# Optimization experiments

Hardware: AMD Instinct MI355X
Metric: run time of the kernel (lower is better)

Reference implementation:

```python
import jax, jax.numpy as jnp
import numpy as np

N_BITS = 8
N_LEVELS = 2 ** N_BITS  # 256
MAX_ITERS = 10
BIG = 3.0e38  # stand-in for +inf that stays finite in fp32


def _init_scales(x):
    """Replicates init_quantization_scale: iteratively peel off 3-sigma outliers.
    Returns per-iteration (thresholds, deltas, zero_points, valid) arrays of
    length MAX_ITERS; `valid[i]` marks iterations that actually recorded a group
    (torch's `break` on empty non-zero set)."""
    xf = x.reshape(-1)

    def step(carry, _):
        xc, done = carry
        absx = jnp.abs(xc)
        nz = xc != 0.0
        n = jnp.sum(nz)
        active = jnp.logical_and(jnp.logical_not(done), n > 0)
        nf = jnp.maximum(n, 1).astype(xc.dtype)
        # mean / unbiased variance of |non-zero elements| (torch .mean()/.var())
        mean = jnp.sum(jnp.where(nz, absx, 0.0)) / nf
        var = jnp.sum(jnp.where(nz, (absx - mean) ** 2, 0.0)) / jnp.maximum(nf - 1.0, 1.0)
        thr = mean + 3.0 * jnp.sqrt(var)
        max_abs = jnp.max(absx)
        # if thr > max: inliers = non-zero elements; else inliers = ~outliers (zeros included)
        inlier = jnp.where(thr > max_abs, nz, absx <= thr)
        x_min = jnp.min(jnp.where(inlier, xc, jnp.asarray(BIG, xc.dtype)))
        x_max = jnp.max(jnp.where(inlier, xc, jnp.asarray(-BIG, xc.dtype)))
        delta = (x_max - x_min) / (N_LEVELS - 1)
        zp = jnp.round(-x_min / delta)
        # keep only outliers for the next iteration
        xc_next = jnp.where(active, jnp.where(absx > thr, xc, 0.0), xc)
        done_next = jnp.logical_or(done, n == 0)
        return (xc_next, done_next), (thr, delta, zp, active)

    (_, _), (thrs, deltas, zps, valids) = jax.lax.scan(
        step, (xf, jnp.asarray(False)), None, length=MAX_ITERS)
    return thrs, deltas, zps, valids


def _dequant(x, thrs, deltas, zps, valids):
    absx = jnp.abs(x)
    # group index: band i is (thr[i-1], thr[i]]; band 0 contributes 0 as in torch
    gi = jnp.zeros(x.shape, dtype=jnp.int32)
    for i in range(1, MAX_ITERS):  # static, small loop over groups
        band = (absx > thrs[i - 1]) & (absx <= thrs[i]) & valids[i]
        gi = gi + band.astype(jnp.int32) * i
    n_groups = jnp.sum(valids.astype(jnp.int32))
    gi = jnp.clip(gi, 0, jnp.maximum(n_groups - 1, 0))
    d = deltas[gi]   # per-element scale
    z = zps[gi]      # per-element zero point
    x_q = jnp.clip(jnp.round(x / d) + z, 0.0, float(N_LEVELS - 1))
    return (x_q - z) * d


def setup_inputs() -> dict:
    key = jax.random.key(0)
    x = jax.random.normal(key, (4, 4096, 4096), dtype=jnp.float32)
    return {"x": x}


def reference(x):
    thrs, deltas, zps, valids = _init_scales(x)
    return _dequant(x, thrs, deltas, zps, valids)
```

## Files before the change

kernel.cpp:

```cpp
#include <hip/hip_runtime.h>

#define BIGF 3.402823466e38f
#define LCAP 2048u
#define NB   2048
#define NT   256

typedef float f32x4 __attribute__((ext_vector_type(4)));

struct State {
  double sum0, sumsq0;
  double sum1, sumsq1;
  double sum2, sumsq2;
  unsigned n0, n1, n2;
  float maxabs0, minnz0, maxnz0;
  float maxabs1, minnz1, maxnz1;
  float maxabs2, minnz2, maxnz2;
  float bmin0, bmax0;
  float bmin1, bmax1;
  unsigned count1, count2;
  float thr0f, thr1f;
  int special0;
  float thr[10], delta[10], zp[10];
  int valid[10];
};

__device__ inline void atomicMinF(float* addr, float v) {
  unsigned* ua = (unsigned*)addr;
  unsigned cur = *ua;
  while (v < __uint_as_float(cur)) {
    unsigned prev = atomicCAS(ua, cur, __float_as_uint(v));
    if (prev == cur) break;
    cur = prev;
  }
}
__device__ inline void atomicMaxF(float* addr, float v) {
  unsigned* ua = (unsigned*)addr;
  unsigned cur = *ua;
  while (v > __uint_as_float(cur)) {
    unsigned prev = atomicCAS(ua, cur, __float_as_uint(v));
    if (prev == cur) break;
    cur = prev;
  }
}

struct Acc8 {
  double sum, sumsq;
  unsigned cnt;
  float maxabs, minnz, maxnz, bmin, bmax;
};
__device__ inline void acc_init(Acc8& a) {
  a.sum = 0.0; a.sumsq = 0.0; a.cnt = 0u;
  a.maxabs = 0.0f;
  a.minnz = BIGF; a.maxnz = -BIGF;
  a.bmin = BIGF; a.bmax = -BIGF;
}
__device__ inline void acc_merge(Acc8& a, const Acc8& b) {
  a.sum += b.sum; a.sumsq += b.sumsq; a.cnt += b.cnt;
  a.maxabs = fmaxf(a.maxabs, b.maxabs);
  a.minnz = fminf(a.minnz, b.minnz); a.maxnz = fmaxf(a.maxnz, b.maxnz);
  a.bmin = fminf(a.bmin, b.bmin);   a.bmax = fmaxf(a.bmax, b.bmax);
}
__device__ inline void acc_wave_reduce(Acc8& a) {
  #pragma unroll
  for (int off = 32; off > 0; off >>= 1) {
    a.sum    += __shfl_down(a.sum, off);
    a.sumsq  += __shfl_down(a.sumsq, off);
    a.cnt    += __shfl_down(a.cnt, off);
    a.maxabs = fmaxf(a.maxabs, __shfl_down(a.maxabs, off));
    a.minnz  = fminf(a.minnz,  __shfl_down(a.minnz, off));
    a.maxnz  = fmaxf(a.maxnz,  __shfl_down(a.maxnz, off));
    a.bmin   = fminf(a.bmin,   __shfl_down(a.bmin, off));
    a.bmax   = fmaxf(a.bmax,   __shfl_down(a.bmax, off));
  }
}
template <int NWAVES>
__device__ inline bool acc_block_reduce(Acc8& a, Acc8* s_part) {
  __syncthreads();
  acc_wave_reduce(a);
  int tid = threadIdx.x;
  if ((tid & 63) == 0) s_part[tid >> 6] = a;
  __syncthreads();
  if (tid == 0) {
    #pragma unroll
    for (int w = 1; w < NWAVES; ++w) acc_merge(a, s_part[w]);
    return true;
  }
  return false;
}

__device__ inline float compute_thr(double sum, double sumsq, unsigned n) {
  double nf = (double)(n > 0u ? n : 1u);
  double mean = sum / nf;
  double nm1 = nf - 1.0; if (nm1 < 1.0) nm1 = 1.0;
  double var = (sumsq - sum * sum / nf) / nm1;
  if (var < 0.0) var = 0.0;
  return (float)(mean + 3.0 * sqrt(var));
}

__device__ inline void finalize_group(float thr, float maxabs, unsigned n,
                                      float minnz, float maxnz, float bmin, float bmax,
                                      bool clampZero, float* dOut, float* zOut, int* vOut) {
  float xmin, xmax;
  if (thr > maxabs) { xmin = minnz; xmax = maxnz; }
  else {
    xmin = bmin; xmax = bmax;
    if (clampZero) { xmin = fminf(xmin, 0.0f); xmax = fmaxf(xmax, 0.0f); }
  }
  float d = (xmax - xmin) / 255.0f;
  int v = (n > 0u) ? 1 : 0;
  float z;
  if (v && d > 0.0f && d < BIGF) { z = rintf((-xmin) / d); }
  else { d = 1.0f; z = 0.0f; }
  *dOut = d; *zOut = z; *vOut = v;
}

__device__ inline void stat1(float f, Acc8& a) {
  float ab = fabsf(f);
  bool nz = (f != 0.0f);
  a.cnt += nz ? 1u : 0u;
  double dab = (double)ab;
  a.sum += dab; a.sumsq += dab * dab;
  a.maxabs = fmaxf(a.maxabs, ab);
  a.minnz = fminf(a.minnz, nz ? f : BIGF);
  a.maxnz = fmaxf(a.maxnz, nz ? f : -BIGF);
}

__global__ void __launch_bounds__(256) k1_stats(const float* __restrict__ x, long long n,
                                                Acc8* __restrict__ part) {
  __shared__ Acc8 s_part[4];
  Acc8 a[4];
  #pragma unroll
  for (int u = 0; u < 4; ++u) acc_init(a[u]);
  const f32x4* x4 = (const f32x4*)x;
  long long n4 = n >> 2;
  long long tid = (long long)blockIdx.x * NT + threadIdx.x;
  long long nthreads = (long long)gridDim.x * NT;
  long long step = nthreads * 8;
  long long nfull = (n4 / step) * step;
  for (long long i = (long long)blockIdx.x * (NT * 8) + threadIdx.x; i < nfull; i += step) {
    f32x4 v[8];
    #pragma unroll
    for (int u = 0; u < 8; ++u) v[u] = x4[i + u * NT];
    #pragma unroll
    for (int u = 0; u < 8; ++u) {
      stat1(v[u].x, a[u & 3]); stat1(v[u].y, a[u & 3]);
      stat1(v[u].z, a[u & 3]); stat1(v[u].w, a[u & 3]);
    }
  }
  for (long long i = nfull + tid; i < n4; i += nthreads) {
    f32x4 v = x4[i];
    stat1(v.x, a[0]); stat1(v.y, a[0]); stat1(v.z, a[0]); stat1(v.w, a[0]);
  }
  for (long long i = (n4 << 2) + tid; i < n; i += nthreads) stat1(x[i], a[0]);

  acc_merge(a[0], a[1]); acc_merge(a[2], a[3]); acc_merge(a[0], a[2]);
  if (acc_block_reduce<4>(a[0], s_part)) part[blockIdx.x] = a[0];
}

__global__ void __launch_bounds__(1024) k1r_reduce(State* st, const Acc8* __restrict__ part, int np) {
  __shared__ Acc8 s_part[16];
  Acc8 a; acc_init(a);
  for (int j = threadIdx.x; j < np; j += 1024) acc_merge(a, part[j]);
  if (acc_block_reduce<16>(a, s_part)) {
    st->sum0 = a.sum; st->sumsq0 = a.sumsq; st->n0 = a.cnt;
    st->maxabs0 = a.maxabs; st->minnz0 = a.minnz; st->maxnz0 = a.maxnz;
    float t = compute_thr(a.sum, a.sumsq, a.cnt);
    st->thr0f = t;
    st->special0 = (t > a.maxabs) ? 1 : 0;
    st->count1 = 0u; st->count2 = 0u;
    st->bmin1 = BIGF; st->bmax1 = -BIGF;
    st->sum2 = 0.0; st->sumsq2 = 0.0; st->n2 = 0u;
    st->maxabs2 = a.maxabs; st->minnz2 = BIGF; st->maxnz2 = -BIGF;
  }
}

__device__ inline void proc2(float f, unsigned idx, float thr0, bool special, Acc8& a,
                             unsigned* l_cnt, float2* l_buf,
                             State* st, float2* __restrict__ buf1, unsigned cap1) {
  float ab = fabsf(f);
  bool out = ab > thr0;
  bool inl = special ? (f != 0.0f) : (!out);
  a.bmin = fminf(a.bmin, inl ? f : BIGF);
  a.bmax = fmaxf(a.bmax, inl ? f : -BIGF);
  a.cnt += out ? 1u : 0u;
  double dab = out ? (double)ab : 0.0;
  a.sum += dab; a.sumsq += dab * dab;
  a.minnz = fminf(a.minnz, out ? f : BIGF);
  a.maxnz = fmaxf(a.maxnz, out ? f : -BIGF);
  unsigned long long m = __ballot(out);
  if (m) {
    unsigned lo = (unsigned)m, hi = (unsigned)(m >> 32);
    int pw = (int)__builtin_amdgcn_mbcnt_hi(hi, __builtin_amdgcn_mbcnt_lo(lo, 0u));
    int nout = __builtin_popcountll(m);
    int leader = __builtin_ctzll(m);
    unsigned bbase = 0u;
    if ((int)(threadIdx.x & 63) == leader) bbase = atomicAdd(l_cnt, (unsigned)nout);
    bbase = (unsigned)__shfl((int)bbase, leader);
    if (out) {
      unsigned p = bbase + (unsigned)pw;
      float2 rec = make_float2(f, __uint_as_float(idx));
      if (p < LCAP) l_buf[p] = rec;
      else { unsigned g = atomicAdd(&st->count1, 1u); if (g < cap1) buf1[g] = rec; }
    }
  }
}

__global__ void __launch_bounds__(256) k2_pass(const float* __restrict__ x, long long n, State* st,
                                               float2* __restrict__ buf1, unsigned cap1,
                                               Acc8* __restrict__ part) {
  __shared__ Acc8 s_part[4];
  __shared__ float2 l_buf[LCAP];
  __shared__ unsigned l_cnt, l_base, l_m;
  if (threadIdx.x == 0) l_cnt = 0u;
  __syncthreads();

  float thr0 = st->thr0f;
  bool special = st->special0 != 0;

  Acc8 a0, a1; acc_init(a0); acc_init(a1);
  const f32x4* x4 = (const f32x4*)x;
  long long n4 = n >> 2;
  long long tid = (long long)blockIdx.x * NT + threadIdx.x;
  long long nthreads = (long long)gridDim.x * NT;
  long long step = nthreads * 4;
  long long nfull = (n4 / step) * step;
  for (long long i = (long long)blockIdx.x * (NT * 4) + threadIdx.x; i < nfull; i += step) {
    f32x4 v0 = x4[i];
    f32x4 v1 = x4[i + NT];
    f32x4 v2 = x4[i + 2 * NT];
    f32x4 v3 = x4[i + 3 * NT];
    unsigned b0 = (unsigned)(i) << 2, b1 = (unsigned)(i + NT) << 2,
             b2 = (unsigned)(i + 2 * NT) << 2, b3 = (unsigned)(i + 3 * NT) << 2;
    proc2(v0.x, b0 + 0u, thr0, special, a0, &l_cnt, l_buf, st, buf1, cap1);
    proc2(v0.y, b0 + 1u, thr0, special, a0, &l_cnt, l_buf, st, buf1, cap1);
    proc2(v0.z, b0 + 2u, thr0, special, a0, &l_cnt, l_buf, st, buf1, cap1);
    proc2(v0.w, b0 + 3u, thr0, special, a0, &l_cnt, l_buf, st, buf1, cap1);
    proc2(v1.x, b1 + 0u, thr0, special, a0, &l_cnt, l_buf, st, buf1, cap1);
    proc2(v1.y, b1 + 1u, thr0, special, a0, &l_cnt, l_buf, st, buf1, cap1);
    proc2(v1.z, b1 + 2u, thr0, special, a0, &l_cnt, l_buf, st, buf1, cap1);
    proc2(v1.w, b1 + 3u, thr0, special, a0, &l_cnt, l_buf, st, buf1, cap1);
    proc2(v2.x, b2 + 0u, thr0, special, a1, &l_cnt, l_buf, st, buf1, cap1);
    proc2(v2.y, b2 + 1u, thr0, special, a1, &l_cnt, l_buf, st, buf1, cap1);
    proc2(v2.z, b2 + 2u, thr0, special, a1, &l_cnt, l_buf, st, buf1, cap1);
    proc2(v2.w, b2 + 3u, thr0, special, a1, &l_cnt, l_buf, st, buf1, cap1);
    proc2(v3.x, b3 + 0u, thr0, special, a1, &l_cnt, l_buf, st, buf1, cap1);
    proc2(v3.y, b3 + 1u, thr0, special, a1, &l_cnt, l_buf, st, buf1, cap1);
    proc2(v3.z, b3 + 2u, thr0, special, a1, &l_cnt, l_buf, st, buf1, cap1);
    proc2(v3.w, b3 + 3u, thr0, special, a1, &l_cnt, l_buf, st, buf1, cap1);
  }
  for (long long i = nfull + tid; i < n4; i += nthreads) {
    f32x4 v = x4[i];
    unsigned b = (unsigned)(i) << 2;
    proc2(v.x, b + 0u, thr0, special, a0, &l_cnt, l_buf, st, buf1, cap1);
    proc2(v.y, b + 1u, thr0, special, a0, &l_cnt, l_buf, st, buf1, cap1);
    proc2(v.z, b + 2u, thr0, special, a0, &l_cnt, l_buf, st, buf1, cap1);
    proc2(v.w, b + 3u, thr0, special, a0, &l_cnt, l_buf, st, buf1, cap1);
  }
  for (long long i = (n4 << 2) + tid; i < n; i += nthreads) {
    proc2(x[i], (unsigned)i, thr0, special, a0, &l_cnt, l_buf, st, buf1, cap1);
  }

  __syncthreads();
  if (threadIdx.x == 0) {
    l_m = l_cnt < LCAP ? l_cnt : LCAP;
    l_base = atomicAdd(&st->count1, l_m);
  }
  __syncthreads();
  for (unsigned i = threadIdx.x; i < l_m; i += NT) {
    unsigned g = l_base + i;
    if (g < cap1) buf1[g] = l_buf[i];
  }
  acc_merge(a0, a1);
  if (acc_block_reduce<4>(a0, s_part)) part[blockIdx.x] = a0;
}

__global__ void __launch_bounds__(1024) k2r_reduce(State* st, const Acc8* __restrict__ part, int np) {
  __shared__ Acc8 s_part[16];
  Acc8 a; acc_init(a);
  for (int j = threadIdx.x; j < np; j += 1024) acc_merge(a, part[j]);
  if (acc_block_reduce<16>(a, s_part)) {
    st->bmin0 = a.bmin; st->bmax0 = a.bmax;
    st->sum1 = a.sum; st->sumsq1 = a.sumsq; st->n1 = a.cnt;
    st->maxabs1 = st->maxabs0;
    st->minnz1 = a.minnz; st->maxnz1 = a.maxnz;
    st->thr1f = compute_thr(a.sum, a.sumsq, a.cnt);
  }
}

__global__ void __launch_bounds__(256) k3_pass(State* st, const float2* __restrict__ buf1, unsigned cap1,
                                               float* __restrict__ buf2, unsigned cap2) {
  __shared__ Acc8 s_part[4];
  __shared__ float l_buf[LCAP];
  __shared__ unsigned l_cnt, l_base, l_m;
  if (threadIdx.x == 0) l_cnt = 0u;
  __syncthreads();

  unsigned c1 = st->count1; if (c1 > cap1) c1 = cap1;
  float thr1 = st->thr1f;

  Acc8 a; acc_init(a);
  unsigned stride = gridDim.x * blockDim.x;
  for (unsigned j = blockIdx.x * blockDim.x + threadIdx.x; j < c1; j += stride) {
    float f = buf1[j].x;
    float ab = fabsf(f);
    if (ab <= thr1) { a.bmin = fminf(a.bmin, f); a.bmax = fmaxf(a.bmax, f); }
    else {
      a.cnt++; a.sum += (double)ab; a.sumsq += (double)ab * (double)ab;
      a.minnz = fminf(a.minnz, f); a.maxnz = fmaxf(a.maxnz, f);
      unsigned p = atomicAdd(&l_cnt, 1u);
      if (p < LCAP) l_buf[p] = f;
      else { unsigned g = atomicAdd(&st->count2, 1u); if (g < cap2) buf2[g] = f; }
    }
  }
  __syncthreads();
  if (threadIdx.x == 0) {
    l_m = l_cnt < LCAP ? l_cnt : LCAP;
    l_base = atomicAdd(&st->count2, l_m);
  }
  __syncthreads();
  for (unsigned i = threadIdx.x; i < l_m; i += blockDim.x) {
    unsigned g = l_base + i;
    if (g < cap2) buf2[g] = l_buf[i];
  }
  if (acc_block_reduce<4>(a, s_part)) {
    atomicMinF(&st->bmin1, a.bmin); atomicMaxF(&st->bmax1, a.bmax);
    atomicAdd(&st->sum2, a.sum); atomicAdd(&st->sumsq2, a.sumsq); atomicAdd(&st->n2, a.cnt);
    atomicMinF(&st->minnz2, a.minnz); atomicMaxF(&st->maxnz2, a.maxnz);
  }
}

__global__ void __launch_bounds__(1024) k4_finalize(State* st, const float* __restrict__ buf2, unsigned cap2) {
  __shared__ Acc8 s_part[16];
  __shared__ float sh_thr[10], sh_delta[10], sh_zp[10];
  __shared__ int sh_valid[10];
  __shared__ double sh_sum, sh_sumsq;
  __shared__ unsigned sh_n;
  __shared__ float sh_maxabs, sh_minnz, sh_maxnz;
  int tid = threadIdx.x;

  if (tid == 0) {
    float thr0 = compute_thr(st->sum0, st->sumsq0, st->n0);
    sh_thr[0] = thr0;
    finalize_group(thr0, st->maxabs0, st->n0, st->minnz0, st->maxnz0,
                   st->bmin0, st->bmax0, false,
                   &sh_delta[0], &sh_zp[0], &sh_valid[0]);
    float thr1 = compute_thr(st->sum1, st->sumsq1, st->n1);
    sh_thr[1] = thr1;
    finalize_group(thr1, st->maxabs1, st->n1, st->minnz1, st->maxnz1,
                   st->bmin1, st->bmax1, true,
                   &sh_delta[1], &sh_zp[1], &sh_valid[1]);
    sh_sum = st->sum2; sh_sumsq = st->sumsq2; sh_n = st->n2;
    sh_maxabs = st->maxabs2; sh_minnz = st->minnz2; sh_maxnz = st->maxnz2;
  }
  __syncthreads();
  unsigned c2 = st->count2; if (c2 > cap2) c2 = cap2;

  for (int i = 2; i < 10; ++i) {
    if (tid == 0) sh_thr[i] = compute_thr(sh_sum, sh_sumsq, sh_n);
    __syncthreads();
    float tp = sh_thr[i - 1], tc = sh_thr[i];
    Acc8 a; acc_init(a);
    for (unsigned j = tid; j < c2; j += 1024u) {
      float f = buf2[j];
      float ab = fabsf(f);
      if (ab > tp && ab <= tc) { a.bmin = fminf(a.bmin, f); a.bmax = fmaxf(a.bmax, f); }
      if (ab > tc) {
        a.cnt++; a.sum += (double)ab; a.sumsq += (double)ab * (double)ab;
        a.maxabs = fmaxf(a.maxabs, ab);
        a.minnz = fminf(a.minnz, f); a.maxnz = fmaxf(a.maxnz, f);
      }
    }
    if (acc_block_reduce<16>(a, s_part)) {
      finalize_group(tc, sh_maxabs, sh_n, sh_minnz, sh_maxnz, a.bmin, a.bmax,
                     true, &sh_delta[i], &sh_zp[i], &sh_valid[i]);
      if (sh_n > 0u) {
        sh_sum = a.sum; sh_sumsq = a.sumsq; sh_n = a.cnt;
        sh_maxabs = a.maxabs; sh_minnz = a.minnz; sh_maxnz = a.maxnz;
      }
    }
    __syncthreads();
  }
  if (tid < 10) {
    st->thr[tid] = sh_thr[tid]; st->delta[tid] = sh_delta[tid];
    st->zp[tid] = sh_zp[tid];   st->valid[tid] = sh_valid[tid];
  }
}

__device__ inline float dq0(float v, float d0, float z0) {
  float q = rintf(v / d0) + z0;
  q = fminf(fmaxf(q, 0.0f), 255.0f);
  return (q - z0) * d0;
}

__global__ void __launch_bounds__(256) k5_dequant(const float* __restrict__ x, float* __restrict__ out,
                                                  long long n, const State* __restrict__ st) {
  float d0 = st->delta[0], z0 = st->zp[0];
  const f32x4* x4 = (const f32x4*)x;
  f32x4* o4 = (f32x4*)out;
  long long n4 = n >> 2;
  long long tid = (long long)blockIdx.x * NT + threadIdx.x;
  long long nthreads = (long long)gridDim.x * NT;
  long long step = nthreads * 8;
  long long nfull = (n4 / step) * step;
  for (long long i = (long long)blockIdx.x * (NT * 8) + threadIdx.x; i < nfull; i += step) {
    f32x4 v[8];
    #pragma unroll
    for (int u = 0; u < 8; ++u) v[u] = x4[i + u * NT];
    #pragma unroll
    for (int u = 0; u < 8; ++u) {
      f32x4 o;
      o.x = dq0(v[u].x, d0, z0);
      o.y = dq0(v[u].y, d0, z0);
      o.z = dq0(v[u].z, d0, z0);
      o.w = dq0(v[u].w, d0, z0);
      __builtin_nontemporal_store(o, &o4[i + u * NT]);
    }
  }
  for (long long i = nfull + tid; i < n4; i += nthreads) {
    f32x4 v = x4[i];
    f32x4 o;
    o.x = dq0(v.x, d0, z0); o.y = dq0(v.y, d0, z0);
    o.z = dq0(v.z, d0, z0); o.w = dq0(v.w, d0, z0);
    o4[i] = o;
  }
  for (long long i = (n4 << 2) + tid; i < n; i += nthreads) {
    out[i] = dq0(x[i], d0, z0);
  }
}

__device__ inline float dq1(float v, const float* thr, const float* dl, const float* zp, const int* vld) {
  float ab = fabsf(v);
  float d = dl[0], z = zp[0];
  #pragma unroll
  for (int i = 1; i < 10; ++i) {
    bool band = (vld[i] != 0) && (ab > thr[i - 1]) && (ab <= thr[i]);
    d = band ? dl[i] : d;
    z = band ? zp[i] : z;
  }
  float q = rintf(v / d) + z;
  q = fminf(fmaxf(q, 0.0f), 255.0f);
  return (q - z) * d;
}

__global__ void __launch_bounds__(256) k6_outliers(const float2* __restrict__ buf1, unsigned cap1,
                                                   float* __restrict__ out, const State* __restrict__ st) {
  unsigned c1 = st->count1; if (c1 > cap1) c1 = cap1;
  float thr[10], dl[10], zp[10]; int vld[10];
  #pragma unroll
  for (int i = 0; i < 10; ++i) {
    thr[i] = st->thr[i]; dl[i] = st->delta[i]; zp[i] = st->zp[i]; vld[i] = st->valid[i];
  }
  unsigned stride = gridDim.x * blockDim.x;
  for (unsigned j = blockIdx.x * blockDim.x + threadIdx.x; j < c1; j += stride) {
    float2 rec = buf1[j];
    out[__float_as_uint(rec.y)] = dq1(rec.x, thr, dl, zp, vld);
  }
}

extern "C" void kernel_launch(void* const* d_in, const int* in_sizes, int n_in,
                              void* d_out, int out_size, void* d_ws, size_t ws_size,
                              hipStream_t stream) {
  const float* x = (const float*)d_in[0];
  float* out = (float*)d_out;
  long long n = (long long)in_sizes[0];

  char* p = (char*)d_ws;
  State* st = (State*)p;            p += 4096;
  Acc8* part1 = (Acc8*)p;           p += (size_t)NB * sizeof(Acc8);
  Acc8* part2 = (Acc8*)p;           p += (size_t)NB * sizeof(Acc8);
  size_t used = (size_t)(p - (char*)d_ws);
  used = (used + 255) & ~(size_t)255;
  size_t avail = ws_size > used ? ws_size - used : 0;
  size_t cap2_sz = avail / 8;
  if (cap2_sz > (size_t)(1u << 20) * 4) cap2_sz = (size_t)(1u << 20) * 4;
  unsigned cap2 = (unsigned)(cap2_sz / 4);
  float* buf2 = (float*)((char*)d_ws + used);
  float2* buf1 = (float2*)(buf2 + cap2);
  unsigned cap1 = (unsigned)((avail - (size_t)cap2 * 4) / 8);

  hipLaunchKernelGGL(k1_stats,    dim3(NB),  dim3(NT),   0, stream, x, n, part1);
  hipLaunchKernelGGL(k1r_reduce,  dim3(1),   dim3(1024), 0, stream, st, (const Acc8*)part1, NB);
  hipLaunchKernelGGL(k2_pass,     dim3(NB),  dim3(NT),   0, stream, x, n, st, buf1, cap1, part2);
  hipLaunchKernelGGL(k2r_reduce,  dim3(1),   dim3(1024), 0, stream, st, (const Acc8*)part2, NB);
  hipLaunchKernelGGL(k3_pass,     dim3(256), dim3(NT),   0, stream, st, (const float2*)buf1, cap1, buf2, cap2);
  hipLaunchKernelGGL(k4_finalize, dim3(1),   dim3(1024), 0, stream, st, (const float*)buf2, cap2);
  hipLaunchKernelGGL(k5_dequant,  dim3(NB),  dim3(NT),   0, stream, x, out, n, st);
  hipLaunchKernelGGL(k6_outliers, dim3(512), dim3(NT),   0, stream, (const float2*)buf1, cap1, out, st);
}
```

Baseline: 676.6 us.

## Fuse first two passes via sampled speculative threshold with fallback pass

The first stats pass now estimates a conservative threshold from a local sample in each block. It captures every element above that estimate into a compact buffer while also collecting inlier min/max, which removes the second full read of the input. If the true threshold falls below any block's estimate, or the buffer overflows, a fallback kernel redoes the full pass. The outlier scatter kernel is folded into the dequant kernel through a wave-uniform fast/slow path. Index-carrying records shrink to plain floats. The cost is extra ballot/LDS work in the first pass and a correctness dependence on the speculative threshold check.

```diff
diff --git a/kernel.cpp b/kernel.cpp
--- a/kernel.cpp
+++ b/kernel.cpp
@@ -17,9 +17,12 @@
   float maxabs2, minnz2, maxnz2;
   float bmin0, bmax0;
   float bmin1, bmax1;
-  unsigned count1, count2;
-  float thr0f, thr1f;
+  unsigned countA;
+  unsigned count1;
+  unsigned count2;
+  float thr0f;
   int special0;
+  int fallback;
   float thr[10], delta[10], zp[10];
   int valid[10];
 };
@@ -48,6 +51,8 @@
   unsigned cnt;
   float maxabs, minnz, maxnz, bmin, bmax;
 };
+struct AccP { Acc8 a; float tspec; };
+
 __device__ inline void acc_init(Acc8& a) {
   a.sum = 0.0; a.sumsq = 0.0; a.cnt = 0u;
   a.maxabs = 0.0f;
@@ -114,7 +119,13 @@
   *dOut = d; *zOut = z; *vOut = v;
 }
 
-__device__ inline void stat1(float f, Acc8& a) {
+__global__ void k0_init(State* st) {
+  if (threadIdx.x == 0 && blockIdx.x == 0) st->countA = 0u;
+}
+
+__device__ inline void proc1(float f, float tspec, Acc8& a,
+                             unsigned* l_cnt, float* l_buf,
+                             State* st, float* __restrict__ bufA, unsigned capA) {
   float ab = fabsf(f);
   bool nz = (f != 0.0f);
   a.cnt += nz ? 1u : 0u;
@@ -123,70 +134,9 @@
   a.maxabs = fmaxf(a.maxabs, ab);
   a.minnz = fminf(a.minnz, nz ? f : BIGF);
   a.maxnz = fmaxf(a.maxnz, nz ? f : -BIGF);
-}
-
-__global__ void __launch_bounds__(256) k1_stats(const float* __restrict__ x, long long n,
-                                                Acc8* __restrict__ part) {
-  __shared__ Acc8 s_part[4];
-  Acc8 a[4];
-  #pragma unroll
-  for (int u = 0; u < 4; ++u) acc_init(a[u]);
-  const f32x4* x4 = (const f32x4*)x;
-  long long n4 = n >> 2;
-  long long tid = (long long)blockIdx.x * NT + threadIdx.x;
-  long long nthreads = (long long)gridDim.x * NT;
-  long long step = nthreads * 8;
-  long long nfull = (n4 / step) * step;
-  for (long long i = (long long)blockIdx.x * (NT * 8) + threadIdx.x; i < nfull; i += step) {
-    f32x4 v[8];
-    #pragma unroll
-    for (int u = 0; u < 8; ++u) v[u] = x4[i + u * NT];
-    #pragma unroll
-    for (int u = 0; u < 8; ++u) {
-      stat1(v[u].x, a[u & 3]); stat1(v[u].y, a[u & 3]);
-      stat1(v[u].z, a[u & 3]); stat1(v[u].w, a[u & 3]);
-    }
-  }
-  for (long long i = nfull + tid; i < n4; i += nthreads) {
-    f32x4 v = x4[i];
-    stat1(v.x, a[0]); stat1(v.y, a[0]); stat1(v.z, a[0]); stat1(v.w, a[0]);
-  }
-  for (long long i = (n4 << 2) + tid; i < n; i += nthreads) stat1(x[i], a[0]);
-
-  acc_merge(a[0], a[1]); acc_merge(a[2], a[3]); acc_merge(a[0], a[2]);
-  if (acc_block_reduce<4>(a[0], s_part)) part[blockIdx.x] = a[0];
-}
-
-__global__ void __launch_bounds__(1024) k1r_reduce(State* st, const Acc8* __restrict__ part, int np) {
-  __shared__ Acc8 s_part[16];
-  Acc8 a; acc_init(a);
-  for (int j = threadIdx.x; j < np; j += 1024) acc_merge(a, part[j]);
-  if (acc_block_reduce<16>(a, s_part)) {
-    st->sum0 = a.sum; st->sumsq0 = a.sumsq; st->n0 = a.cnt;
-    st->maxabs0 = a.maxabs; st->minnz0 = a.minnz; st->maxnz0 = a.maxnz;
-    float t = compute_thr(a.sum, a.sumsq, a.cnt);
-    st->thr0f = t;
-    st->special0 = (t > a.maxabs) ? 1 : 0;
-    st->count1 = 0u; st->count2 = 0u;
-    st->bmin1 = BIGF; st->bmax1 = -BIGF;
-    st->sum2 = 0.0; st->sumsq2 = 0.0; st->n2 = 0u;
-    st->maxabs2 = a.maxabs; st->minnz2 = BIGF; st->maxnz2 = -BIGF;
-  }
-}
-
-__device__ inline void proc2(float f, unsigned idx, float thr0, bool special, Acc8& a,
-                             unsigned* l_cnt, float2* l_buf,
-                             State* st, float2* __restrict__ buf1, unsigned cap1) {
-  float ab = fabsf(f);
-  bool out = ab > thr0;
-  bool inl = special ? (f != 0.0f) : (!out);
-  a.bmin = fminf(a.bmin, inl ? f : BIGF);
-  a.bmax = fmaxf(a.bmax, inl ? f : -BIGF);
-  a.cnt += out ? 1u : 0u;
-  double dab = out ? (double)ab : 0.0;
-  a.sum += dab; a.sumsq += dab * dab;
-  a.minnz = fminf(a.minnz, out ? f : BIGF);
-  a.maxnz = fmaxf(a.maxnz, out ? f : -BIGF);
+  bool out = ab > tspec;
+  a.bmin = fminf(a.bmin, out ? BIGF : f);
+  a.bmax = fmaxf(a.bmax, out ? -BIGF : f);
   unsigned long long m = __ballot(out);
   if (m) {
     unsigned lo = (unsigned)m, hi = (unsigned)(m >> 32);
@@ -198,68 +148,194 @@
     bbase = (unsigned)__shfl((int)bbase, leader);
     if (out) {
       unsigned p = bbase + (unsigned)pw;
-      float2 rec = make_float2(f, __uint_as_float(idx));
-      if (p < LCAP) l_buf[p] = rec;
-      else { unsigned g = atomicAdd(&st->count1, 1u); if (g < cap1) buf1[g] = rec; }
-    }
-  }
-}
-
-__global__ void __launch_bounds__(256) k2_pass(const float* __restrict__ x, long long n, State* st,
-                                               float2* __restrict__ buf1, unsigned cap1,
-                                               Acc8* __restrict__ part) {
+      if (p < LCAP) l_buf[p] = f;
+      else { unsigned g = atomicAdd(&st->countA, 1u); if (g < capA) bufA[g] = f; }
+    }
+  }
+}
+
+__global__ void __launch_bounds__(256) k1_stats(const float* __restrict__ x, long long n,
+                                                AccP* __restrict__ part,
+                                                float* __restrict__ bufA, unsigned capA,
+                                                State* st) {
   __shared__ Acc8 s_part[4];
-  __shared__ float2 l_buf[LCAP];
+  __shared__ float l_buf[LCAP];
+  __shared__ unsigned l_cnt, l_base, l_m;
+  __shared__ float s_s[4], s_ss[4], s_c[4], s_tspec;
+  int tid = threadIdx.x;
+  if (tid == 0) l_cnt = 0u;
+
+  const f32x4* x4 = (const f32x4*)x;
+  long long n4 = n >> 2;
+  long long gtid = (long long)blockIdx.x * NT + tid;
+  long long nthreads = (long long)gridDim.x * NT;
+  long long step = nthreads * 8;
+  long long nfull = (n4 / step) * step;
+  long long i0 = (long long)blockIdx.x * (NT * 8) + tid;
+
+  {
+    float s = 0.0f, ss = 0.0f; unsigned c = 0u;
+    #pragma unroll
+    for (int u = 0; u < 2; ++u) {
+      long long i = i0 + u * NT;
+      if (i < n4) {
+        f32x4 v = x4[i];
+        float e[4] = {v.x, v.y, v.z, v.w};
+        #pragma unroll
+        for (int k = 0; k < 4; ++k) {
+          float ab = fabsf(e[k]);
+          c += (ab != 0.0f) ? 1u : 0u;
+          s += ab; ss += ab * ab;
+        }
+      }
+    }
+    #pragma unroll
+    for (int off = 32; off > 0; off >>= 1) {
+      s  += __shfl_down(s, off);
+      ss += __shfl_down(ss, off);
+      c  += __shfl_down(c, off);
+    }
+    if ((tid & 63) == 0) { s_s[tid >> 6] = s; s_ss[tid >> 6] = ss; s_c[tid >> 6] = (float)c; }
+    __syncthreads();
+    if (tid == 0) {
+      float S = s_s[0] + s_s[1] + s_s[2] + s_s[3];
+      float SS = s_ss[0] + s_ss[1] + s_ss[2] + s_ss[3];
+      float C = s_c[0] + s_c[1] + s_c[2] + s_c[3];
+      float nf = C > 1.0f ? C : 1.0f;
+      float m = S / nf;
+      float var = (SS - S * S / nf) / fmaxf(nf - 1.0f, 1.0f);
+      var = fmaxf(var, 0.0f);
+      s_tspec = 0.8f * (m + 3.0f * sqrtf(var));
+    }
+    __syncthreads();
+  }
+  float tspec = s_tspec;
+
+  Acc8 a0, a1; acc_init(a0); acc_init(a1);
+  for (long long i = i0; i < nfull; i += step) {
+    f32x4 v[8];
+    #pragma unroll
+    for (int u = 0; u < 8; ++u) v[u] = x4[i + u * NT];
+    #pragma unroll
+    for (int u = 0; u < 8; ++u) {
+      Acc8& a = (u & 1) ? a1 : a0;
+      proc1(v[u].x, tspec, a, &l_cnt, l_buf, st, bufA, capA);
+      proc1(v[u].y, tspec, a, &l_cnt, l_buf, st, bufA, capA);
+      proc1(v[u].z, tspec, a, &l_cnt, l_buf, st, bufA, capA);
+      proc1(v[u].w, tspec, a, &l_cnt, l_buf, st, bufA, capA);
+    }
+  }
+  for (long long i = nfull + gtid; i < n4; i += nthreads) {
+    f32x4 v = x4[i];
+    proc1(v.x, tspec, a0, &l_cnt, l_buf, st, bufA, capA);
+    proc1(v.y, tspec, a0, &l_cnt, l_buf, st, bufA, capA);
+    proc1(v.z, tspec, a0, &l_cnt, l_buf, st, bufA, capA);
+    proc1(v.w, tspec, a0, &l_cnt, l_buf, st, bufA, capA);
+  }
+  for (long long i = (n4 << 2) + gtid; i < n; i += nthreads) {
+    proc1(x[i], tspec, a0, &l_cnt, l_buf, st, bufA, capA);
+  }
+
+  __syncthreads();
+  if (tid == 0) {
+    l_m = l_cnt < LCAP ? l_cnt : LCAP;
+    l_base = atomicAdd(&st->countA, l_m);
+  }
+  __syncthreads();
+  for (unsigned i = tid; i < l_m; i += NT) {
+    unsigned g = l_base + i;
+    if (g < capA) bufA[g] = l_buf[i];
+  }
+  acc_merge(a0, a1);
+  if (acc_block_reduce<4>(a0, s_part)) { part[blockIdx.x].a = a0; part[blockIdx.x].tspec = tspec; }
+}
+
+__global__ void __launch_bounds__(1024) k1r_reduce(State* st, const AccP* __restrict__ part,
+                                                   int np, unsigned capA) {
+  __shared__ Acc8 s_part[16];
+  __shared__ float s_tm[16];
+  Acc8 a; acc_init(a);
+  float tm = 0.0f;
+  for (int j = threadIdx.x; j < np; j += 1024) {
+    acc_merge(a, part[j].a);
+    tm = fmaxf(tm, part[j].tspec);
+  }
+  #pragma unroll
+  for (int off = 32; off > 0; off >>= 1) tm = fmaxf(tm, __shfl_down(tm, off));
+  if ((threadIdx.x & 63) == 0) s_tm[threadIdx.x >> 6] = tm;
+  if (acc_block_reduce<16>(a, s_part)) {
+    #pragma unroll
+    for (int w = 1; w < 16; ++w) tm = fmaxf(tm, s_tm[w]);
+    st->sum0 = a.sum; st->sumsq0 = a.sumsq; st->n0 = a.cnt;
+    st->maxabs0 = a.maxabs; st->minnz0 = a.minnz; st->maxnz0 = a.maxnz;
+    float t = compute_thr(a.sum, a.sumsq, a.cnt);
+    st->thr0f = t;
+    st->special0 = (t > a.maxabs) ? 1 : 0;
+    unsigned cA = st->countA;
+    bool ok = (tm <= t) && (cA <= capA);
+    st->fallback = ok ? 0 : 1;
+    st->bmin0 = ok ? a.bmin : BIGF;
+    st->bmax0 = ok ? a.bmax : -BIGF;
+    st->count1 = 0u; st->count2 = 0u;
+    st->sum1 = 0.0; st->sumsq1 = 0.0; st->n1 = 0u;
+    st->maxabs1 = a.maxabs;
+    st->minnz1 = BIGF; st->maxnz1 = -BIGF;
+    st->bmin1 = BIGF; st->bmax1 = -BIGF;
+    st->sum2 = 0.0; st->sumsq2 = 0.0; st->n2 = 0u;
+    st->maxabs2 = a.maxabs;
+    st->minnz2 = BIGF; st->maxnz2 = -BIGF;
+  }
+}
+
+__global__ void __launch_bounds__(256) k2_full(const float* __restrict__ x, long long n, State* st,
+                                               float* __restrict__ bufB, unsigned capB) {
+  if (st->fallback == 0) return;
+  __shared__ Acc8 s_part[4];
+  __shared__ float l_buf[LCAP];
   __shared__ unsigned l_cnt, l_base, l_m;
   if (threadIdx.x == 0) l_cnt = 0u;
   __syncthreads();
 
   float thr0 = st->thr0f;
   bool special = st->special0 != 0;
-
-  Acc8 a0, a1; acc_init(a0); acc_init(a1);
+  Acc8 a; acc_init(a);
   const f32x4* x4 = (const f32x4*)x;
   long long n4 = n >> 2;
-  long long tid = (long long)blockIdx.x * NT + threadIdx.x;
+  long long gtid = (long long)blockIdx.x * NT + threadIdx.x;
   long long nthreads = (long long)gridDim.x * NT;
-  long long step = nthreads * 4;
-  long long nfull = (n4 / step) * step;
-  for (long long i = (long long)blockIdx.x * (NT * 4) + threadIdx.x; i < nfull; i += step) {
-    f32x4 v0 = x4[i];
-    f32x4 v1 = x4[i + NT];
-    f32x4 v2 = x4[i + 2 * NT];
-    f32x4 v3 = x4[i + 3 * NT];
-    unsigned b0 = (unsigned)(i) << 2, b1 = (unsigned)(i + NT) << 2,
-             b2 = (unsigned)(i + 2 * NT) << 2, b3 = (unsigned)(i + 3 * NT) << 2;
-    proc2(v0.x, b0 + 0u, thr0, special, a0, &l_cnt, l_buf, st, buf1, cap1);
-    proc2(v0.y, b0 + 1u, thr0, special, a0, &l_cnt, l_buf, st, buf1, cap1);
-    proc2(v0.z, b0 + 2u, thr0, special, a0, &l_cnt, l_buf, st, buf1, cap1);
-    proc2(v0.w, b0 + 3u, thr0, special, a0, &l_cnt, l_buf, st, buf1, cap1);
-    proc2(v1.x, b1 + 0u, thr0, special, a0, &l_cnt, l_buf, st, buf1, cap1);
-    proc2(v1.y, b1 + 1u, thr0, special, a0, &l_cnt, l_buf, st, buf1, cap1);
-    proc2(v1.z, b1 + 2u, thr0, special, a0, &l_cnt, l_buf, st, buf1, cap1);
-    proc2(v1.w, b1 + 3u, thr0, special, a0, &l_cnt, l_buf, st, buf1, cap1);
-    proc2(v2.x, b2 + 0u, thr0, special, a1, &l_cnt, l_buf, st, buf1, cap1);
-    proc2(v2.y, b2 + 1u, thr0, special, a1, &l_cnt, l_buf, st, buf1, cap1);
-    proc2(v2.z, b2 + 2u, thr0, special, a1, &l_cnt, l_buf, st, buf1, cap1);
-    proc2(v2.w, b2 + 3u, thr0, special, a1, &l_cnt, l_buf, st, buf1, cap1);
-    proc2(v3.x, b3 + 0u, thr0, special, a1, &l_cnt, l_buf, st, buf1, cap1);
-    proc2(v3.y, b3 + 1u, thr0, special, a1, &l_cnt, l_buf, st, buf1, cap1);
-    proc2(v3.z, b3 + 2u, thr0, special, a1, &l_cnt, l_buf, st, buf1, cap1);
-    proc2(v3.w, b3 + 3u, thr0, special, a1, &l_cnt, l_buf, st, buf1, cap1);
-  }
-  for (long long i = nfull + tid; i < n4; i += nthreads) {
+  for (long long i = gtid; i < n4; i += nthreads) {
     f32x4 v = x4[i];
-    unsigned b = (unsigned)(i) << 2;
-    proc2(v.x, b + 0u, thr0, special, a0, &l_cnt, l_buf, st, buf1, cap1);
-    proc2(v.y, b + 1u, thr0, special, a0, &l_cnt, l_buf, st, buf1, cap1);
-    proc2(v.z, b + 2u, thr0, special, a0, &l_cnt, l_buf, st, buf1, cap1);
-    proc2(v.w, b + 3u, thr0, special, a0, &l_cnt, l_buf, st, buf1, cap1);
-  }
-  for (long long i = (n4 << 2) + tid; i < n; i += nthreads) {
-    proc2(x[i], (unsigned)i, thr0, special, a0, &l_cnt, l_buf, st, buf1, cap1);
-  }
-
+    float e[4] = {v.x, v.y, v.z, v.w};
+    #pragma unroll
+    for (int k = 0; k < 4; ++k) {
+      float f = e[k];
+      float ab = fabsf(f);
+      bool out = ab > thr0;
+      bool inl = special ? (f != 0.0f) : (!out);
+      if (inl) { a.bmin = fminf(a.bmin, f); a.bmax = fmaxf(a.bmax, f); }
+      if (out) {
+        a.cnt++; a.sum += (double)ab; a.sumsq += (double)ab * (double)ab;
+        a.minnz = fminf(a.minnz, f); a.maxnz = fmaxf(a.maxnz, f);
+        unsigned p = atomicAdd(&l_cnt, 1u);
+        if (p < LCAP) l_buf[p] = f;
+        else { unsigned g = atomicAdd(&st->count1, 1u); if (g < capB) bufB[g] = f; }
+      }
+    }
+  }
+  for (long long i = (n4 << 2) + gtid; i < n; i += nthreads) {
+    float f = x[i];
+    float ab = fabsf(f);
+    bool out = ab > thr0;
+    bool inl = special ? (f != 0.0f) : (!out);
+    if (inl) { a.bmin = fminf(a.bmin, f); a.bmax = fmaxf(a.bmax, f); }
+    if (out) {
+      a.cnt++; a.sum += (double)ab; a.sumsq += (double)ab * (double)ab;
+      a.minnz = fminf(a.minnz, f); a.maxnz = fmaxf(a.maxnz, f);
+      unsigned p = atomicAdd(&l_cnt, 1u);
+      if (p < LCAP) l_buf[p] = f;
+      else { unsigned g = atomicAdd(&st->count1, 1u); if (g < capB) bufB[g] = f; }
+    }
+  }
   __syncthreads();
   if (threadIdx.x == 0) {
     l_m = l_cnt < LCAP ? l_cnt : LCAP;
@@ -268,26 +344,77 @@
   __syncthreads();
   for (unsigned i = threadIdx.x; i < l_m; i += NT) {
     unsigned g = l_base + i;
-    if (g < cap1) buf1[g] = l_buf[i];
-  }
-  acc_merge(a0, a1);
-  if (acc_block_reduce<4>(a0, s_part)) part[blockIdx.x] = a0;
-}
-
-__global__ void __launch_bounds__(1024) k2r_reduce(State* st, const Acc8* __restrict__ part, int np) {
-  __shared__ Acc8 s_part[16];
+    if (g < capB) bufB[g] = l_buf[i];
+  }
+  if (acc_block_reduce<4>(a, s_part)) {
+    atomicMinF(&st->bmin0, a.bmin); atomicMaxF(&st->bmax0, a.bmax);
+    atomicAdd(&st->sum1, a.sum); atomicAdd(&st->sumsq1, a.sumsq); atomicAdd(&st->n1, a.cnt);
+    atomicMinF(&st->minnz1, a.minnz); atomicMaxF(&st->maxnz1, a.maxnz);
+  }
+}
+
+__global__ void __launch_bounds__(256) k2c_pass(State* st, const float* __restrict__ bufA, unsigned capA,
+                                                float* __restrict__ bufB, unsigned capB) {
+  if (st->fallback != 0) return;
+  __shared__ Acc8 s_part[4];
+  __shared__ float l_buf[LCAP];
+  __shared__ unsigned l_cnt, l_base, l_m;
+  if (threadIdx.x == 0) l_cnt = 0u;
+  __syncthreads();
+
+  unsigned cA = st->countA; if (cA > capA) cA = capA;
+  float thr0 = st->thr0f;
   Acc8 a; acc_init(a);
-  for (int j = threadIdx.x; j < np; j += 1024) acc_merge(a, part[j]);
-  if (acc_block_reduce<16>(a, s_part)) {
-    st->bmin0 = a.bmin; st->bmax0 = a.bmax;
-    st->sum1 = a.sum; st->sumsq1 = a.sumsq; st->n1 = a.cnt;
-    st->maxabs1 = st->maxabs0;
-    st->minnz1 = a.minnz; st->maxnz1 = a.maxnz;
-    st->thr1f = compute_thr(a.sum, a.sumsq, a.cnt);
-  }
-}
-
-__global__ void __launch_bounds__(256) k3_pass(State* st, const float2* __restrict__ buf1, unsigned cap1,
+  unsigned stride = gridDim.x * blockDim.x;
+  unsigned cA4 = cA >> 2;
+  const f32x4* bufA4 = (const f32x4*)bufA;
+  for (unsigned j = blockIdx.x * blockDim.x + threadIdx.x; j < cA4; j += stride) {
+    f32x4 v = bufA4[j];
+    float e[4] = {v.x, v.y, v.z, v.w};
+    #pragma unroll
+    for (int k = 0; k < 4; ++k) {
+      float f = e[k];
+      float ab = fabsf(f);
+      if (ab <= thr0) { a.bmin = fminf(a.bmin, f); a.bmax = fmaxf(a.bmax, f); }
+      else {
+        a.cnt++; a.sum += (double)ab; a.sumsq += (double)ab * (double)ab;
+        a.minnz = fminf(a.minnz, f); a.maxnz = fmaxf(a.maxnz, f);
+        unsigned p = atomicAdd(&l_cnt, 1u);
+        if (p < LCAP) l_buf[p] = f;
+        else { unsigned g = atomicAdd(&st->count1, 1u); if (g < capB) bufB[g] = f; }
+      }
+    }
+  }
+  for (unsigned j = (cA4 << 2) + blockIdx.x * blockDim.x + threadIdx.x; j < cA; j += stride) {
+    float f = bufA[j];
+    float ab = fabsf(f);
+    if (ab <= thr0) { a.bmin = fminf(a.bmin, f); a.bmax = fmaxf(a.bmax, f); }
+    else {
+      a.cnt++; a.sum += (double)ab; a.sumsq += (double)ab * (double)ab;
+      a.minnz = fminf(a.minnz, f); a.maxnz = fmaxf(a.maxnz, f);
+      unsigned p = atomicAdd(&l_cnt, 1u);
+      if (p < LCAP) l_buf[p] = f;
+      else { unsigned g = atomicAdd(&st->count1, 1u); if (g < capB) bufB[g] = f; }
+    }
+  }
+  __syncthreads();
+  if (threadIdx.x == 0) {
+    l_m = l_cnt < LCAP ? l_cnt : LCAP;
+    l_base = atomicAdd(&st->count1, l_m);
+  }
+  __syncthreads();
+  for (unsigned i = threadIdx.x; i < l_m; i += NT) {
+    unsigned g = l_base + i;
+    if (g < capB) bufB[g] = l_buf[i];
+  }
+  if (acc_block_reduce<4>(a, s_part)) {
+    atomicMinF(&st->bmin0, a.bmin); atomicMaxF(&st->bmax0, a.bmax);
+    atomicAdd(&st->sum1, a.sum); atomicAdd(&st->sumsq1, a.sumsq); atomicAdd(&st->n1, a.cnt);
+    atomicMinF(&st->minnz1, a.minnz); atomicMaxF(&st->maxnz1, a.maxnz);
+  }
+}
+
+__global__ void __launch_bounds__(256) k3_pass(State* st, const float* __restrict__ bufB, unsigned capB,
                                                float* __restrict__ buf2, unsigned cap2) {
   __shared__ Acc8 s_part[4];
   __shared__ float l_buf[LCAP];
@@ -295,13 +422,13 @@
   if (threadIdx.x == 0) l_cnt = 0u;
   __syncthreads();
 
-  unsigned c1 = st->count1; if (c1 > cap1) c1 = cap1;
-  float thr1 = st->thr1f;
+  unsigned c1 = st->count1; if (c1 > capB) c1 = capB;
+  float thr1 = compute_thr(st->sum1, st->sumsq1, st->n1);
 
   Acc8 a; acc_init(a);
   unsigned stride = gridDim.x * blockDim.x;
   for (unsigned j = blockIdx.x * blockDim.x + threadIdx.x; j < c1; j += stride) {
-    float f = buf1[j].x;
+    float f = bufB[j];
     float ab = fabsf(f);
     if (ab <= thr1) { a.bmin = fminf(a.bmin, f); a.bmax = fmaxf(a.bmax, f); }
     else {
@@ -391,43 +518,6 @@
   q = fminf(fmaxf(q, 0.0f), 255.0f);
   return (q - z0) * d0;
 }
-
-__global__ void __launch_bounds__(256) k5_dequant(const float* __restrict__ x, float* __restrict__ out,
-                                                  long long n, const State* __restrict__ st) {
-  float d0 = st->delta[0], z0 = st->zp[0];
-  const f32x4* x4 = (const f32x4*)x;
-  f32x4* o4 = (f32x4*)out;
-  long long n4 = n >> 2;
-  long long tid = (long long)blockIdx.x * NT + threadIdx.x;
-  long long nthreads = (long long)gridDim.x * NT;
-  long long step = nthreads * 8;
-  long long nfull = (n4 / step) * step;
-  for (long long i = (long long)blockIdx.x * (NT * 8) + threadIdx.x; i < nfull; i += step) {
-    f32x4 v[8];
-    #pragma unroll
-    for (int u = 0; u < 8; ++u) v[u] = x4[i + u * NT];
-    #pragma unroll
-    for (int u = 0; u < 8; ++u) {
-      f32x4 o;
-      o.x = dq0(v[u].x, d0, z0);
-      o.y = dq0(v[u].y, d0, z0);
-      o.z = dq0(v[u].z, d0, z0);
-      o.w = dq0(v[u].w, d0, z0);
-      __builtin_nontemporal_store(o, &o4[i + u * NT]);
-    }
-  }
-  for (long long i = nfull + tid; i < n4; i += nthreads) {
-    f32x4 v = x4[i];
-    f32x4 o;
-    o.x = dq0(v.x, d0, z0); o.y = dq0(v.y, d0, z0);
-    o.z = dq0(v.z, d0, z0); o.w = dq0(v.w, d0, z0);
-    o4[i] = o;
-  }
-  for (long long i = (n4 << 2) + tid; i < n; i += nthreads) {
-    out[i] = dq0(x[i], d0, z0);
-  }
-}
-
 __device__ inline float dq1(float v, const float* thr, const float* dl, const float* zp, const int* vld) {
   float ab = fabsf(v);
   float d = dl[0], z = zp[0];
@@ -441,19 +531,52 @@
   q = fminf(fmaxf(q, 0.0f), 255.0f);
   return (q - z) * d;
 }
-
-__global__ void __launch_bounds__(256) k6_outliers(const float2* __restrict__ buf1, unsigned cap1,
-                                                   float* __restrict__ out, const State* __restrict__ st) {
-  unsigned c1 = st->count1; if (c1 > cap1) c1 = cap1;
+__device__ inline float dq(float v, float t0, float d0, float z0,
+                           const float* thr, const float* dl, const float* zp, const int* vld) {
+  if (__any(fabsf(v) > t0)) return dq1(v, thr, dl, zp, vld);
+  return dq0(v, d0, z0);
+}
+
+__global__ void __launch_bounds__(256) k5_dequant(const float* __restrict__ x, float* __restrict__ out,
+                                                  long long n, const State* __restrict__ st) {
   float thr[10], dl[10], zp[10]; int vld[10];
   #pragma unroll
   for (int i = 0; i < 10; ++i) {
     thr[i] = st->thr[i]; dl[i] = st->delta[i]; zp[i] = st->zp[i]; vld[i] = st->valid[i];
   }
-  unsigned stride = gridDim.x * blockDim.x;
-  for (unsigned j = blockIdx.x * blockDim.x + threadIdx.x; j < c1; j += stride) {
-    float2 rec = buf1[j];
-    out[__float_as_uint(rec.y)] = dq1(rec.x, thr, dl, zp, vld);
+  float d0 = dl[0], z0 = zp[0], t0 = thr[0];
+  const f32x4* x4 = (const f32x4*)x;
+  f32x4* o4 = (f32x4*)out;
+  long long n4 = n >> 2;
+  long long gtid = (long long)blockIdx.x * NT + threadIdx.x;
+  long long nthreads = (long long)gridDim.x * NT;
+  long long step = nthreads * 8;
+  long long nfull = (n4 / step) * step;
+  for (long long i = (long long)blockIdx.x * (NT * 8) + threadIdx.x; i < nfull; i += step) {
+    f32x4 v[8];
+    #pragma unroll
+    for (int u = 0; u < 8; ++u) v[u] = __builtin_nontemporal_load(&x4[i + u * NT]);
+    #pragma unroll
+    for (int u = 0; u < 8; ++u) {
+      f32x4 o;
+      o.x = dq(v[u].x, t0, d0, z0, thr, dl, zp, vld);
+      o.y = dq(v[u].y, t0, d0, z0, thr, dl, zp, vld);
+      o.z = dq(v[u].z, t0, d0, z0, thr, dl, zp, vld);
+      o.w = dq(v[u].w, t0, d0, z0, thr, dl, zp, vld);
+      __builtin_nontemporal_store(o, &o4[i + u * NT]);
+    }
+  }
+  for (long long i = nfull + gtid; i < n4; i += nthreads) {
+    f32x4 v = x4[i];
+    f32x4 o;
+    o.x = dq(v.x, t0, d0, z0, thr, dl, zp, vld);
+    o.y = dq(v.y, t0, d0, z0, thr, dl, zp, vld);
+    o.z = dq(v.z, t0, d0, z0, thr, dl, zp, vld);
+    o.w = dq(v.w, t0, d0, z0, thr, dl, zp, vld);
+    o4[i] = o;
+  }
+  for (long long i = (n4 << 2) + gtid; i < n; i += nthreads) {
+    out[i] = dq(x[i], t0, d0, z0, thr, dl, zp, vld);
   }
 }
 
@@ -466,24 +589,26 @@
 
   char* p = (char*)d_ws;
   State* st = (State*)p;            p += 4096;
-  Acc8* part1 = (Acc8*)p;           p += (size_t)NB * sizeof(Acc8);
-  Acc8* part2 = (Acc8*)p;           p += (size_t)NB * sizeof(Acc8);
+  AccP* part = (AccP*)p;            p += (size_t)NB * sizeof(AccP);
   size_t used = (size_t)(p - (char*)d_ws);
   used = (used + 255) & ~(size_t)255;
   size_t avail = ws_size > used ? ws_size - used : 0;
-  size_t cap2_sz = avail / 8;
-  if (cap2_sz > (size_t)(1u << 20) * 4) cap2_sz = (size_t)(1u << 20) * 4;
-  unsigned cap2 = (unsigned)(cap2_sz / 4);
+  size_t b2_sz = (avail / 16) & ~(size_t)255;
+  size_t bB_sz = (avail / 4) & ~(size_t)255;
+  size_t bA_sz = avail - b2_sz - bB_sz;
   float* buf2 = (float*)((char*)d_ws + used);
-  float2* buf1 = (float2*)(buf2 + cap2);
-  unsigned cap1 = (unsigned)((avail - (size_t)cap2 * 4) / 8);
-
-  hipLaunchKernelGGL(k1_stats,    dim3(NB),  dim3(NT),   0, stream, x, n, part1);
-  hipLaunchKernelGGL(k1r_reduce,  dim3(1),   dim3(1024), 0, stream, st, (const Acc8*)part1, NB);
-  hipLaunchKernelGGL(k2_pass,     dim3(NB),  dim3(NT),   0, stream, x, n, st, buf1, cap1, part2);
-  hipLaunchKernelGGL(k2r_reduce,  dim3(1),   dim3(1024), 0, stream, st, (const Acc8*)part2, NB);
-  hipLaunchKernelGGL(k3_pass,     dim3(256), dim3(NT),   0, stream, st, (const float2*)buf1, cap1, buf2, cap2);
+  float* bufB = (float*)((char*)buf2 + b2_sz);
+  float* bufA = (float*)((char*)bufB + bB_sz);
+  unsigned cap2 = (unsigned)(b2_sz / 4);
+  unsigned capB = (unsigned)(bB_sz / 4);
+  unsigned capA = (unsigned)(bA_sz / 4);
+
+  hipLaunchKernelGGL(k0_init,     dim3(1),   dim3(64),   0, stream, st);
+  hipLaunchKernelGGL(k1_stats,    dim3(NB),  dim3(NT),   0, stream, x, n, part, bufA, capA, st);
+  hipLaunchKernelGGL(k1r_reduce,  dim3(1),   dim3(1024), 0, stream, st, (const AccP*)part, NB, capA);
+  hipLaunchKernelGGL(k2_full,     dim3(NB),  dim3(NT),   0, stream, x, n, st, bufB, capB);
+  hipLaunchKernelGGL(k2c_pass,    dim3(512), dim3(NT),   0, stream, st, (const float*)bufA, capA, bufB, capB);
+  hipLaunchKernelGGL(k3_pass,     dim3(256), dim3(NT),   0, stream, st, (const float*)bufB, capB, buf2, cap2);
   hipLaunchKernelGGL(k4_finalize, dim3(1),   dim3(1024), 0, stream, st, (const float*)buf2, cap2);
   hipLaunchKernelGGL(k5_dequant,  dim3(NB),  dim3(NT),   0, stream, x, out, n, st);
-  hipLaunchKernelGGL(k6_outliers, dim3(512), dim3(NT),   0, stream, (const float2*)buf1, cap1, out, st);
-}
+}
```

After: 688.6 us. Within noise of the previous version (+1.8%).
